# Kernel optimization log

Measured on AMD Instinct MI355X. Metric: run time of the kernel, lower is better.

## Reference

```python
import jax, jax.numpy as jnp
import numpy as np

B, D, H, O = 4096, 1024, 8192, 1000

def setup_inputs() -> dict:
    key = jax.random.key(0)
    k1, k2, k3 = jax.random.split(key, 3)
    x = jax.random.normal(k1, (B, D), dtype=jnp.float32)
    kohonen_weights = jax.random.normal(k2, (H, D), dtype=jnp.float32) * (6.0 / (H + D)) ** 0.5
    grossberg_weights = jax.random.normal(k3, (O, H), dtype=jnp.float32) * (6.0 / (O + H)) ** 0.5
    return {"x": x, "kohonen_weights": kohonen_weights, "grossberg_weights": grossberg_weights}

def reference(x, kohonen_weights, grossberg_weights):
    # but kept faithful since distances only feed argmin -> same winners either way)
    x_sq = jnp.sum(x * x, axis=1, keepdims=True)                      # [B,1]
    w_sq = jnp.sum(kohonen_weights * kohonen_weights, axis=1)         # [H]
    sq_dists = x_sq - 2.0 * (x @ kohonen_weights.T) + w_sq[None, :]   # [B,H]
    winners = jnp.argmin(sq_dists, axis=1)                            # [B]
    # one_hot @ grossberg.T is mathematically a row gather of grossberg.T
    output = grossberg_weights.T[winners]                             # [B,O]
    return output, winners
```

## Files before the change

kernel.cpp:

```cpp
#include <hip/hip_runtime.h>
#include <hip/hip_bf16.h>

#define B_ 4096
#define D_ 1024
#define H_ 8192
#define O_ 1000
#define K2 2048
#define NT 48

typedef __attribute__((ext_vector_type(8))) short short8;
typedef __attribute__((ext_vector_type(4))) short short4v;
typedef __attribute__((ext_vector_type(4))) float f32x4;

union BF4 { __hip_bfloat16 b[4]; short4v s; };

__device__ __forceinline__ void gload16(void* ldsp, const void* g) {
  __builtin_amdgcn_global_load_lds(
      (const __attribute__((address_space(1))) unsigned int*)g,
      (__attribute__((address_space(3))) unsigned int*)ldsp, 16, 0, 0);
}

__device__ __forceinline__ int aoff_(int T) {
  const int t = T / 3, r = T - 3 * t;
  return (r == 1 ? 1024 : 0) + t * 64;
}
__device__ __forceinline__ int boff_(int T) {
  const int t = T / 3, r = T - 3 * t;
  return (r == 2 ? 1024 : 0) + t * 64;
}

__global__ __launch_bounds__(256) void split_rows_kernel(
    const float* __restrict__ src, __hip_bfloat16* __restrict__ dst,
    float* __restrict__ sq)
{
  const int r = blockIdx.x;
  const int t = threadIdx.x;
  const float4 v = ((const float4*)(src + (size_t)r * D_))[t];
  float ss = v.x * v.x + v.y * v.y + v.z * v.z + v.w * v.w;

  BF4 Hh, Ll;
  const float e[4] = {v.x, v.y, v.z, v.w};
#pragma unroll
  for (int i = 0; i < 4; ++i) {
    __hip_bfloat16 h = __float2bfloat16(e[i]);
    Hh.b[i] = h;
    Ll.b[i] = __float2bfloat16(e[i] - __bfloat162float(h));
  }
  __hip_bfloat16* base = dst + (size_t)r * K2;
  *(short4v*)(base + t * 4) = Hh.s;
  *(short4v*)(base + 1024 + t * 4) = Ll.s;

#pragma unroll
  for (int o = 32; o > 0; o >>= 1) ss += __shfl_down(ss, o);
  __shared__ float wsum[4];
  if ((t & 63) == 0) wsum[t >> 6] = ss;
  __syncthreads();
  if (t == 0) sq[r] = (wsum[0] + wsum[1]) + (wsum[2] + wsum[3]);
}


#define BAR() do { asm volatile("" ::: "memory"); \
                   __builtin_amdgcn_s_barrier(); \
                   asm volatile("" ::: "memory"); } while (0)

#define GATE(tt) do { if ((tt) < NT/2 - 2) asm volatile("s_waitcnt vmcnt(4)" ::: "memory"); \
                      else                 asm volatile("s_waitcnt vmcnt(0)" ::: "memory"); } while (0)

#define STAGE(P, prow, T, isB, h) do { if ((T) < NT) { \
    const int koff_ = (isB) ? boff_(T) : aoff_(T); \
    const __hip_bfloat16* s_ = (P) + (size_t)((prow) + (h)*128 + wid*16 + srow) * K2 + koff_ + sunit * 8; \
    char* d_ = lds + ((T)&1)*65536 + (isB)*32768 + (h)*16384 + wid*2048 + lane*16; \
    gload16(d_, s_); gload16(d_ + 1024, s_ + 8*K2); } } while (0)

#define LOAD_A(dsel, mb) do { \
    const char* pA_ = lds + (dsel) + wm*16384 + (mb)*2048 + aro; \
    _Pragma("unroll") for (int m_ = 0; m_ < 4; ++m_) { \
      af[m_][0] = *(const short8*)(pA_ + m_*2048 + kof0); \
      af[m_][1] = *(const short8*)(pA_ + m_*2048 + kof1); } } while (0)

#define LOAD_B(dsel, nb, dstf) do { \
    const char* pB_ = lds + (dsel) + 32768 + bq + (nb)*2048 + aro; \
    _Pragma("unroll") for (int n_ = 0; n_ < 2; ++n_) { \
      dstf[n_][0] = *(const short8*)(pB_ + n_*2048 + kof0); \
      dstf[n_][1] = *(const short8*)(pB_ + n_*2048 + kof1); } } while (0)

#define MM(accb, bfr, nb) do { \
    __builtin_amdgcn_s_setprio(1); \
    _Pragma("unroll") for (int m_ = 0; m_ < 4; ++m_) \
    _Pragma("unroll") for (int n_ = 0; n_ < 2; ++n_) { \
      acc[(accb)+m_][(nb)+n_] = __builtin_amdgcn_mfma_f32_16x16x32_bf16( \
          af[m_][0], bfr[n_][0], acc[(accb)+m_][(nb)+n_], 0, 0, 0); \
      acc[(accb)+m_][(nb)+n_] = __builtin_amdgcn_mfma_f32_16x16x32_bf16( \
          af[m_][1], bfr[n_][1], acc[(accb)+m_][(nb)+n_], 0, 0, 0); } \
    __builtin_amdgcn_s_setprio(0); } while (0)

__global__ __launch_bounds__(512, 2) void gemm_argmin_kernel(
    const __hip_bfloat16* __restrict__ Ap, const __hip_bfloat16* __restrict__ Bp,
    const float* __restrict__ xsq, const float* __restrict__ wsq,
    unsigned long long* __restrict__ keys)
{
  __shared__ char lds[131072];

  const int t = threadIdx.x;
  const int id = blockIdx.x;
  const int xcd = id & 7;
  const int r_ = id >> 3;
  const int by = (xcd >> 2) * 8 + (r_ >> 3);
  const int bx = (xcd & 3) * 8 + (r_ & 7);
  const int brow = by * 256, bcol = bx * 256;

  const int lane = t & 63, wid = t >> 6;
  const int wm = wid >> 2, wn = wid & 3;
  const int cc = lane & 15, q = lane >> 4, sw = lane & 7;
  const int aro = cc * 128;
  const int kof0 = (q ^ sw) * 16;
  const int kof1 = ((4 + q) ^ sw) * 16;
  const int bq = (wn >> 1) * 16384 + (wn & 1) * 8192;

  const int srow = lane >> 3;
  const int sunit = (lane & 7) ^ srow;

  f32x4 acc[8][4] = {};
  short8 af[4][2], bf0[2][2], bf1[2][2];

  STAGE(Ap, brow, 0, 0, 0); STAGE(Ap, brow, 0, 0, 1);
  STAGE(Bp, bcol, 0, 1, 0); STAGE(Bp, bcol, 0, 1, 1);
  STAGE(Bp, bcol, 1, 1, 0); STAGE(Ap, brow, 1, 0, 0);
  asm volatile("s_waitcnt vmcnt(4)" ::: "memory");
  __builtin_amdgcn_s_barrier();
  asm volatile("" ::: "memory");

  for (int it = 0; it < NT / 2; ++it) {
    const int T0 = 2 * it, T1 = 2 * it + 1;
    LOAD_A(0, 0); LOAD_B(0, 0, bf0);
    STAGE(Ap, brow, T1, 0, 1);
    BAR();
    MM(0, bf0, 0);
    BAR();
    LOAD_B(0, 2, bf1);
    STAGE(Bp, bcol, T1, 1, 1);
    BAR();
    MM(0, bf1, 2);
    BAR();
    LOAD_A(0, 4);
    STAGE(Bp, bcol, T0 + 2, 1, 0);
    BAR();
    MM(4, bf0, 0);
    BAR();
    STAGE(Ap, brow, T0 + 2, 0, 0);
    BAR();
    MM(4, bf1, 2);
    GATE(it);
    BAR();
    LOAD_A(65536, 0); LOAD_B(65536, 0, bf0);
    STAGE(Ap, brow, T0 + 2, 0, 1);
    BAR();
    MM(0, bf0, 0);
    BAR();
    LOAD_B(65536, 2, bf1);
    STAGE(Bp, bcol, T0 + 2, 1, 1);
    BAR();
    MM(0, bf1, 2);
    BAR();
    LOAD_A(65536, 4);
    STAGE(Bp, bcol, T1 + 2, 1, 0);
    BAR();
    MM(4, bf0, 0);
    BAR();
    STAGE(Ap, brow, T1 + 2, 0, 0);
    BAR();
    MM(4, bf1, 2);
    GATE(it);
    BAR();
  }

#pragma unroll
  for (int m = 0; m < 8; ++m) {
#pragma unroll
    for (int r = 0; r < 4; ++r) {
      const int row = brow + wm * 128 + m * 16 + q * 4 + r;
      const float xs = xsq[row];
      unsigned long long best = ~0ULL;
#pragma unroll
      for (int n = 0; n < 4; ++n) {
        const int col = bcol + wn * 64 + n * 16 + cc;
        const float s = (xs - 2.0f * acc[m][n][r]) + wsq[col];
        unsigned ub = __float_as_uint(s);
        ub = (ub & 0x80000000u) ? ~ub : (ub | 0x80000000u);
        const unsigned long long key =
            ((unsigned long long)ub << 32) | (unsigned)col;
        if (key < best) best = key;
      }
#pragma unroll
      for (int o = 1; o < 16; o <<= 1) {
        const unsigned long long v = __shfl_xor(best, o);
        if (v < best) best = v;
      }
      if (cc == 0) atomicMin(&keys[row], best);
    }
  }
}

__global__ __launch_bounds__(256) void transposeG_kernel(
    const float* __restrict__ G, float* __restrict__ GT)
{
  __shared__ float tile[32][33];
  const int h0 = blockIdx.x * 32;
  const int o0 = blockIdx.y * 32;
  const int tx = threadIdx.x;
  const int ty = threadIdx.y;
#pragma unroll
  for (int j = 0; j < 4; ++j) {
    const int o = o0 + ty + j * 8;
    if (o < O_) tile[ty + j * 8][tx] = G[(size_t)o * H_ + h0 + tx];
  }
  __syncthreads();
  const int o = o0 + tx;
  if (o < O_) {
#pragma unroll
    for (int j = 0; j < 4; ++j)
      GT[(size_t)(h0 + ty + j * 8) * O_ + o] = tile[tx][ty + j * 8];
  }
}

__global__ __launch_bounds__(256) void finalize_kernel(
    const unsigned long long* __restrict__ keys,
    const float* __restrict__ GT, float* __restrict__ out)
{
  const int b = blockIdx.x;
  const unsigned w = (unsigned)(keys[b] & 0xFFFFFFFFull);
  if (threadIdx.x == 0) out[(size_t)B_ * O_ + b] = (float)w;
  const float4* src = (const float4*)(GT + (size_t)w * O_);
  float4* dst = (float4*)(out + (size_t)b * O_);
  for (int i = threadIdx.x; i < O_ / 4; i += 256) dst[i] = src[i];
}

extern "C" void kernel_launch(void* const* d_in, const int* in_sizes, int n_in,
                              void* d_out, int out_size, void* d_ws, size_t ws_size,
                              hipStream_t stream)
{
  (void)in_sizes; (void)n_in; (void)out_size; (void)ws_size;
  const float* x = (const float*)d_in[0];
  const float* kw = (const float*)d_in[1];
  const float* gw = (const float*)d_in[2];
  float* out = (float*)d_out;

  char* ws = (char*)d_ws;
  __hip_bfloat16* Ap = (__hip_bfloat16*)(ws);
  __hip_bfloat16* Bp = (__hip_bfloat16*)(ws + 16777216);
  float* xsq = (float*)(ws + 50331648);
  float* wsq = (float*)(ws + 50331648 + 16384);
  unsigned long long* keys = (unsigned long long*)(ws + 50331648 + 16384 + 32768);
  float* GT = (float*)(ws);

  hipMemsetAsync(keys, 0xFF, B_ * sizeof(unsigned long long), stream);
  split_rows_kernel<<<B_, 256, 0, stream>>>(x, Ap, xsq);
  split_rows_kernel<<<H_, 256, 0, stream>>>(kw, Bp, wsq);
  gemm_argmin_kernel<<<512, 512, 0, stream>>>(Ap, Bp, xsq, wsq, keys);
  transposeG_kernel<<<dim3(H_ / 32, (O_ + 31) / 32), dim3(32, 8), 0, stream>>>(gw, GT);
  finalize_kernel<<<B_, 256, 0, stream>>>(keys, GT, out);
}
```

Before: 250.1 us.

## Restructure GEMM main loop into register double-buffered 4x4 MFMA sub-steps

Rewrites the bf16 GEMM inner loop so each phase reads one K-half of the A and B fragments into alternate register sets (afA/afB, bfA/bfB) while the previous set feeds a 4x4 block of MFMAs. The LDS staging order is rescheduled to match, with sched_barrier hints to stop the compiler reordering. The goal is to hide LDS read latency behind MFMA work and cut the number of block-wide barriers per tile. The cost is more live fragment registers and a stricter vmcnt(0) wait at every gate, and the new buffer reuse pattern risks ordering hazards.

```diff
diff --git a/kernel.cpp b/kernel.cpp
--- a/kernel.cpp
+++ b/kernel.cpp
@@ -7,6 +7,7 @@
 #define O_ 1000
 #define K2 2048
 #define NT 48
+#define NITER (NT / 2)
 
 typedef __attribute__((ext_vector_type(8))) short short8;
 typedef __attribute__((ext_vector_type(4))) short short4v;
@@ -62,9 +63,8 @@
 #define BAR() do { asm volatile("" ::: "memory"); \
                    __builtin_amdgcn_s_barrier(); \
                    asm volatile("" ::: "memory"); } while (0)
-
-#define GATE(tt) do { if ((tt) < NT/2 - 2) asm volatile("s_waitcnt vmcnt(4)" ::: "memory"); \
-                      else                 asm volatile("s_waitcnt vmcnt(0)" ::: "memory"); } while (0)
+#define SB0() __builtin_amdgcn_sched_barrier(0)
+#define GATEV0() asm volatile("s_waitcnt vmcnt(0)" ::: "memory")
 
 #define STAGE(P, prow, T, isB, h) do { if ((T) < NT) { \
     const int koff_ = (isB) ? boff_(T) : aoff_(T); \
@@ -72,26 +72,22 @@
     char* d_ = lds + ((T)&1)*65536 + (isB)*32768 + (h)*16384 + wid*2048 + lane*16; \
     gload16(d_, s_); gload16(d_ + 1024, s_ + 8*K2); } } while (0)
 
-#define LOAD_A(dsel, mb) do { \
-    const char* pA_ = lds + (dsel) + wm*16384 + (mb)*2048 + aro; \
-    _Pragma("unroll") for (int m_ = 0; m_ < 4; ++m_) { \
-      af[m_][0] = *(const short8*)(pA_ + m_*2048 + kof0); \
-      af[m_][1] = *(const short8*)(pA_ + m_*2048 + kof1); } } while (0)
-
-#define LOAD_B(dsel, nb, dstf) do { \
-    const char* pB_ = lds + (dsel) + 32768 + bq + (nb)*2048 + aro; \
-    _Pragma("unroll") for (int n_ = 0; n_ < 2; ++n_) { \
-      dstf[n_][0] = *(const short8*)(pB_ + n_*2048 + kof0); \
-      dstf[n_][1] = *(const short8*)(pB_ + n_*2048 + kof1); } } while (0)
-
-#define MM(accb, bfr, nb) do { \
+#define READ_A(dst, dsel, mh, KOF) do { \
+    const char* p_ = lds + (dsel) + wm*16384 + (mh)*8192 + aro + (KOF); \
+    _Pragma("unroll") for (int m_ = 0; m_ < 4; ++m_) \
+      dst[m_] = *(const short8*)(p_ + m_*2048); } while (0)
+
+#define READ_B(dst, dsel, KOF) do { \
+    const char* p_ = lds + (dsel) + 32768 + bq + aro + (KOF); \
+    _Pragma("unroll") for (int n_ = 0; n_ < 4; ++n_) \
+      dst[n_] = *(const short8*)(p_ + n_*2048); } while (0)
+
+#define MM16(mh, AF, BF) do { \
     __builtin_amdgcn_s_setprio(1); \
     _Pragma("unroll") for (int m_ = 0; m_ < 4; ++m_) \
-    _Pragma("unroll") for (int n_ = 0; n_ < 2; ++n_) { \
-      acc[(accb)+m_][(nb)+n_] = __builtin_amdgcn_mfma_f32_16x16x32_bf16( \
-          af[m_][0], bfr[n_][0], acc[(accb)+m_][(nb)+n_], 0, 0, 0); \
-      acc[(accb)+m_][(nb)+n_] = __builtin_amdgcn_mfma_f32_16x16x32_bf16( \
-          af[m_][1], bfr[n_][1], acc[(accb)+m_][(nb)+n_], 0, 0, 0); } \
+    _Pragma("unroll") for (int n_ = 0; n_ < 4; ++n_) \
+      acc[(mh)*4 + m_][n_] = __builtin_amdgcn_mfma_f32_16x16x32_bf16( \
+          AF[m_], BF[n_], acc[(mh)*4 + m_][n_], 0, 0, 0); \
     __builtin_amdgcn_s_setprio(0); } while (0)
 
 __global__ __launch_bounds__(512, 2) void gemm_argmin_kernel(
@@ -121,56 +117,62 @@
   const int sunit = (lane & 7) ^ srow;
 
   f32x4 acc[8][4] = {};
-  short8 af[4][2], bf0[2][2], bf1[2][2];
+  short8 afA[4], afB[4], bfA[4], bfB[4];
 
   STAGE(Ap, brow, 0, 0, 0); STAGE(Ap, brow, 0, 0, 1);
   STAGE(Bp, bcol, 0, 1, 0); STAGE(Bp, bcol, 0, 1, 1);
-  STAGE(Bp, bcol, 1, 1, 0); STAGE(Ap, brow, 1, 0, 0);
+  STAGE(Bp, bcol, 1, 1, 0); STAGE(Bp, bcol, 1, 1, 1);
   asm volatile("s_waitcnt vmcnt(4)" ::: "memory");
-  __builtin_amdgcn_s_barrier();
-  asm volatile("" ::: "memory");
-
-  for (int it = 0; it < NT / 2; ++it) {
-    const int T0 = 2 * it, T1 = 2 * it + 1;
-    LOAD_A(0, 0); LOAD_B(0, 0, bf0);
-    STAGE(Ap, brow, T1, 0, 1);
-    BAR();
-    MM(0, bf0, 0);
-    BAR();
-    LOAD_B(0, 2, bf1);
-    STAGE(Bp, bcol, T1, 1, 1);
-    BAR();
-    MM(0, bf1, 2);
-    BAR();
-    LOAD_A(0, 4);
-    STAGE(Bp, bcol, T0 + 2, 1, 0);
-    BAR();
-    MM(4, bf0, 0);
-    BAR();
-    STAGE(Ap, brow, T0 + 2, 0, 0);
-    BAR();
-    MM(4, bf1, 2);
-    GATE(it);
-    BAR();
-    LOAD_A(65536, 0); LOAD_B(65536, 0, bf0);
-    STAGE(Ap, brow, T0 + 2, 0, 1);
-    BAR();
-    MM(0, bf0, 0);
-    BAR();
-    LOAD_B(65536, 2, bf1);
-    STAGE(Bp, bcol, T0 + 2, 1, 1);
-    BAR();
-    MM(0, bf1, 2);
-    BAR();
-    LOAD_A(65536, 4);
-    STAGE(Bp, bcol, T1 + 2, 1, 0);
-    BAR();
-    MM(4, bf0, 0);
-    BAR();
-    STAGE(Ap, brow, T1 + 2, 0, 0);
-    BAR();
-    MM(4, bf1, 2);
-    GATE(it);
+  BAR();
+  READ_A(afA, 0, 0, kof0);
+  READ_B(bfA, 0, kof0);
+
+  for (int it = 0; it < NITER; ++it) {
+    const int a = 2 * it, b = 2 * it + 1;
+    STAGE(Ap, brow, b, 0, 0); STAGE(Ap, brow, b, 0, 1);
+    READ_A(afB, 0, 1, kof0);
+    SB0();
+    MM16(0, afA, bfA);
+    BAR();
+    READ_A(afA, 0, 0, kof1);
+    READ_B(bfB, 0, kof1);
+    SB0();
+    MM16(1, afB, bfA);
+    BAR();
+    READ_A(afB, 0, 1, kof1);
+    SB0();
+    MM16(0, afA, bfB);
+    GATEV0();
+    BAR();
+    STAGE(Bp, bcol, a + 2, 1, 0);
+    READ_A(afA, 65536, 0, kof0);
+    READ_B(bfA, 65536, kof0);
+    SB0();
+    MM16(1, afB, bfB);
+    BAR();
+    STAGE(Bp, bcol, a + 2, 1, 1);
+    STAGE(Ap, brow, a + 2, 0, 0); STAGE(Ap, brow, a + 2, 0, 1);
+    READ_A(afB, 65536, 1, kof0);
+    SB0();
+    MM16(0, afA, bfA);
+    BAR();
+    READ_A(afA, 65536, 0, kof1);
+    READ_B(bfB, 65536, kof1);
+    SB0();
+    MM16(1, afB, bfA);
+    BAR();
+    READ_A(afB, 65536, 1, kof1);
+    SB0();
+    MM16(0, afA, bfB);
+    GATEV0();
+    BAR();
+    STAGE(Bp, bcol, b + 2, 1, 0); STAGE(Bp, bcol, b + 2, 1, 1);
+    if (it < NITER - 1) {
+      READ_A(afA, 0, 0, kof0);
+      READ_B(bfA, 0, kof0);
+    }
+    SB0();
+    MM16(1, afB, bfB);
     BAR();
   }
 
```

New measurement: 249.1 us. About the same (-0.4%).
